# Kernel optimization log

Hardware: AMD Instinct MI355X
Metric: run time of the kernel (lower is better)

The kernel has to match this reference:

```python
import jax, jax.numpy as jnp
import numpy as np


def setup_inputs() -> dict:
    key = jax.random.key(0)
    k1, k2 = jax.random.split(key)
    N = 16384
    NUM_ANCHORS = 64
    HIDDEN_DIM = 128
    adj = jax.random.uniform(k1, (N, N), dtype=jnp.float32)
    anchor_emb = jax.random.normal(k2, (NUM_ANCHORS, HIDDEN_DIM), dtype=jnp.float32)
    return {"adj": adj, "anchor_emb": anchor_emb}


def reference(adj, anchor_emb):
    # adj: [N, N], anchor_emb: [A, H]
    num_anchors = anchor_emb.shape[0]
    deg = jnp.sum(adj, axis=-1, keepdims=True)              # [N, 1]
    nrm = jnp.linalg.norm(deg) + 1e-6                       # scalar ||deg||_F
    # sim[:, :A] of (deg @ deg.T)/nrm computed directly without the full NxN product
    sim = (deg * deg[:num_anchors, 0][None, :]) / nrm       # [N, A]
    anchor_weights = jax.nn.softmax(sim, axis=-1)           # [N, A]
    return anchor_weights @ anchor_emb                      # [N, H]
```

## Files before the change

kernel.cpp:

```cpp
#include <hip/hip_runtime.h>


constexpr int N_NODES = 16384;
constexpr int N_ANCH  = 64;
constexpr int HID     = 128;

__global__ __launch_bounds__(256) void rowsum_kernel(const float* __restrict__ adj,
                                                     float* __restrict__ deg) {
    const int row  = blockIdx.x;
    const int t    = threadIdx.x;
    const float4* __restrict__ p =
        reinterpret_cast<const float4*>(adj) + (size_t)row * (N_NODES / 4);

    float s = 0.0f;
#pragma unroll
    for (int i = 0; i < (N_NODES / 4) / 256; ++i) {
        float4 v = p[t + i * 256];
        s += (v.x + v.y) + (v.z + v.w);
    }
#pragma unroll
    for (int off = 32; off > 0; off >>= 1) s += __shfl_down(s, off, 64);

    __shared__ float partial[4];
    const int lane = t & 63, wid = t >> 6;
    if (lane == 0) partial[wid] = s;
    __syncthreads();
    if (t == 0) deg[row] = (partial[0] + partial[1]) + (partial[2] + partial[3]);
}

__global__ __launch_bounds__(1024) void norm_kernel(const float* __restrict__ deg,
                                                    float* __restrict__ nrm) {
    const int t = threadIdx.x;
    float s = 0.0f;
    for (int i = t; i < N_NODES; i += 1024) {
        float d = deg[i];
        s += d * d;
    }
#pragma unroll
    for (int off = 32; off > 0; off >>= 1) s += __shfl_down(s, off, 64);

    __shared__ float partial[16];
    const int lane = t & 63, wid = t >> 6;
    if (lane == 0) partial[wid] = s;
    __syncthreads();
    if (t == 0) {
        float tot = 0.0f;
#pragma unroll
        for (int i = 0; i < 16; ++i) tot += partial[i];
        *nrm = sqrtf(tot) + 1e-6f;
    }
}

__global__ __launch_bounds__(256) void out_kernel(const float* __restrict__ deg,
                                                  const float* __restrict__ nrm,
                                                  const float* __restrict__ emb,
                                                  float* __restrict__ out) {
    __shared__ float s_emb[N_ANCH * HID];
    __shared__ float s_dega[N_ANCH];

    const int t = threadIdx.x;
    for (int i = t; i < N_ANCH * HID; i += 256) s_emb[i] = emb[i];
    if (t < N_ANCH) s_dega[t] = deg[t];
    __syncthreads();

    const float inv_nrm = 1.0f / (*nrm);
    const int wid = t >> 6, lane = t & 63;
    const int rows_per_wave = N_NODES / (gridDim.x * 4);
    const int row0 = (blockIdx.x * 4 + wid) * rows_per_wave;

    for (int r = 0; r < rows_per_wave; ++r) {
        const int row = row0 + r;
        const float d = deg[row];
        const float sim = d * s_dega[lane] * inv_nrm;

        float m = sim;
#pragma unroll
        for (int off = 32; off > 0; off >>= 1) m = fmaxf(m, __shfl_xor(m, off, 64));
        const float e = expf(sim - m);
        float ssum = e;
#pragma unroll
        for (int off = 32; off > 0; off >>= 1) ssum += __shfl_xor(ssum, off, 64);
        const float w = e / ssum;

        float acc0 = 0.0f, acc1 = 0.0f;
#pragma unroll
        for (int a = 0; a < N_ANCH; ++a) {
            const float wa = __shfl(w, a, 64);
            acc0 = fmaf(wa, s_emb[a * HID + lane],      acc0);
            acc1 = fmaf(wa, s_emb[a * HID + 64 + lane], acc1);
        }
        out[(size_t)row * HID + lane]      = acc0;
        out[(size_t)row * HID + 64 + lane] = acc1;
    }
}

extern "C" void kernel_launch(void* const* d_in, const int* in_sizes, int n_in,
                              void* d_out, int out_size, void* d_ws, size_t ws_size,
                              hipStream_t stream) {
    const float* adj = (const float*)d_in[0];
    const float* emb = (const float*)d_in[1];
    float* out = (float*)d_out;

    float* deg = (float*)d_ws;
    float* nrm = deg + N_NODES;

    rowsum_kernel<<<N_NODES, 256, 0, stream>>>(adj, deg);
    norm_kernel<<<1, 1024, 0, stream>>>(deg, nrm);
    out_kernel<<<1024, 256, 0, stream>>>(deg, nrm, emb, out);
}
```

Before: 219.7 us.

## Fuse norm into rowsum and output kernels, wave-per-row nontemporal loads

Removes the single-block norm kernel. The rowsum kernel now writes per-block partial sums of squares, and the output kernel reduces those partials itself. Rowsum is restructured so each wave handles two rows, with 16 outstanding nontemporal float4 loads per batch to raise memory-level parallelism on the 1 GiB adjacency read. The output kernel keeps embedding columns in registers, passes softmax weights through shared memory instead of per-anchor shuffles, and uses fast exp. In exchange, every output block redundantly reduces the 2048 partials, and register pressure rises.

```diff
diff --git a/kernel.cpp b/kernel.cpp
--- a/kernel.cpp
+++ b/kernel.cpp
@@ -4,90 +4,101 @@
 constexpr int N_NODES = 16384;
 constexpr int N_ANCH  = 64;
 constexpr int HID     = 128;
+constexpr int ROWS_PER_BLOCK = 8;
+constexpr int K1_BLOCKS = N_NODES / ROWS_PER_BLOCK;
+constexpr int K3_BLOCKS = 1024;
+
+typedef float f4 __attribute__((ext_vector_type(4)));
 
 __global__ __launch_bounds__(256) void rowsum_kernel(const float* __restrict__ adj,
-                                                     float* __restrict__ deg) {
-    const int row  = blockIdx.x;
-    const int t    = threadIdx.x;
-    const float4* __restrict__ p =
-        reinterpret_cast<const float4*>(adj) + (size_t)row * (N_NODES / 4);
+                                                     float* __restrict__ deg,
+                                                     float* __restrict__ ssq_part) {
+    const int t = threadIdx.x, lane = t & 63, wid = t >> 6;
+    const int row0 = blockIdx.x * ROWS_PER_BLOCK + wid * 2;
+    float ssq = 0.0f;
 
-    float s = 0.0f;
+    for (int r = 0; r < 2; ++r) {
+        const int row = row0 + r;
+        const f4* __restrict__ p =
+            reinterpret_cast<const f4*>(adj) + (size_t)row * (N_NODES / 4) + lane;
+        float s = 0.0f;
+        for (int c = 0; c < 4; ++c) {
+            f4 v[16];
 #pragma unroll
-    for (int i = 0; i < (N_NODES / 4) / 256; ++i) {
-        float4 v = p[t + i * 256];
-        s += (v.x + v.y) + (v.z + v.w);
+            for (int i = 0; i < 16; ++i)
+                v[i] = __builtin_nontemporal_load(p + c * 1024 + i * 64);
+#pragma unroll
+            for (int i = 0; i < 16; ++i)
+                s += (v[i].x + v[i].y) + (v[i].z + v[i].w);
+        }
+#pragma unroll
+        for (int off = 32; off > 0; off >>= 1) s += __shfl_down(s, off, 64);
+        if (lane == 0) { deg[row] = s; ssq = fmaf(s, s, ssq); }
     }
-#pragma unroll
-    for (int off = 32; off > 0; off >>= 1) s += __shfl_down(s, off, 64);
 
-    __shared__ float partial[4];
-    const int lane = t & 63, wid = t >> 6;
-    if (lane == 0) partial[wid] = s;
+    __shared__ float sp[4];
+    if (lane == 0) sp[wid] = ssq;
     __syncthreads();
-    if (t == 0) deg[row] = (partial[0] + partial[1]) + (partial[2] + partial[3]);
-}
-
-__global__ __launch_bounds__(1024) void norm_kernel(const float* __restrict__ deg,
-                                                    float* __restrict__ nrm) {
-    const int t = threadIdx.x;
-    float s = 0.0f;
-    for (int i = t; i < N_NODES; i += 1024) {
-        float d = deg[i];
-        s += d * d;
-    }
-#pragma unroll
-    for (int off = 32; off > 0; off >>= 1) s += __shfl_down(s, off, 64);
-
-    __shared__ float partial[16];
-    const int lane = t & 63, wid = t >> 6;
-    if (lane == 0) partial[wid] = s;
-    __syncthreads();
-    if (t == 0) {
-        float tot = 0.0f;
-#pragma unroll
-        for (int i = 0; i < 16; ++i) tot += partial[i];
-        *nrm = sqrtf(tot) + 1e-6f;
-    }
+    if (t == 0) ssq_part[blockIdx.x] = (sp[0] + sp[1]) + (sp[2] + sp[3]);
 }
 
 __global__ __launch_bounds__(256) void out_kernel(const float* __restrict__ deg,
-                                                  const float* __restrict__ nrm,
+                                                  const float* __restrict__ ssq_part,
                                                   const float* __restrict__ emb,
                                                   float* __restrict__ out) {
     __shared__ float s_emb[N_ANCH * HID];
-    __shared__ float s_dega[N_ANCH];
+    __shared__ float s_w[4][N_ANCH];
+    __shared__ float s_red[4];
+    __shared__ float s_inv;
 
-    const int t = threadIdx.x;
-    for (int i = t; i < N_ANCH * HID; i += 256) s_emb[i] = emb[i];
-    if (t < N_ANCH) s_dega[t] = deg[t];
+    const int t = threadIdx.x, lane = t & 63, wid = t >> 6;
+
+    float ss = 0.0f;
+#pragma unroll
+    for (int i = 0; i < K1_BLOCKS / 256; ++i) ss += ssq_part[t + i * 256];
+#pragma unroll
+    for (int off = 32; off > 0; off >>= 1) ss += __shfl_down(ss, off, 64);
+    if (lane == 0) s_red[wid] = ss;
+
+    for (int i = t; i < N_ANCH * HID / 4; i += 256)
+        reinterpret_cast<f4*>(s_emb)[i] = reinterpret_cast<const f4*>(emb)[i];
     __syncthreads();
+    if (t == 0)
+        s_inv = 1.0f / (sqrtf((s_red[0] + s_red[1]) + (s_red[2] + s_red[3])) + 1e-6f);
+    __syncthreads();
+    const float inv_nrm = s_inv;
 
-    const float inv_nrm = 1.0f / (*nrm);
-    const int wid = t >> 6, lane = t & 63;
-    const int rows_per_wave = N_NODES / (gridDim.x * 4);
-    const int row0 = (blockIdx.x * 4 + wid) * rows_per_wave;
+    float e0[N_ANCH], e1[N_ANCH];
+#pragma unroll
+    for (int a = 0; a < N_ANCH; ++a) {
+        e0[a] = s_emb[a * HID + lane];
+        e1[a] = s_emb[a * HID + 64 + lane];
+    }
 
-    for (int r = 0; r < rows_per_wave; ++r) {
+    const float da = deg[lane] * inv_nrm;
+    const int row0 = (blockIdx.x * 4 + wid) * 4;
+
+    for (int r = 0; r < 4; ++r) {
         const int row = row0 + r;
-        const float d = deg[row];
-        const float sim = d * s_dega[lane] * inv_nrm;
+        const float sim = deg[row] * da;
 
         float m = sim;
 #pragma unroll
         for (int off = 32; off > 0; off >>= 1) m = fmaxf(m, __shfl_xor(m, off, 64));
-        const float e = expf(sim - m);
-        float ssum = e;
+        const float e = __expf(sim - m);
+        float sum = e;
 #pragma unroll
-        for (int off = 32; off > 0; off >>= 1) ssum += __shfl_xor(ssum, off, 64);
-        const float w = e / ssum;
+        for (int off = 32; off > 0; off >>= 1) sum += __shfl_xor(sum, off, 64);
+        s_w[wid][lane] = e / sum;
 
         float acc0 = 0.0f, acc1 = 0.0f;
 #pragma unroll
-        for (int a = 0; a < N_ANCH; ++a) {
-            const float wa = __shfl(w, a, 64);
-            acc0 = fmaf(wa, s_emb[a * HID + lane],      acc0);
-            acc1 = fmaf(wa, s_emb[a * HID + 64 + lane], acc1);
+        for (int a4 = 0; a4 < N_ANCH; a4 += 4) {
+            f4 w4 = *reinterpret_cast<const f4*>(&s_w[wid][a4]);
+            acc0 = fmaf(w4.x, e0[a4 + 0], acc0); acc1 = fmaf(w4.x, e1[a4 + 0], acc1);
+            acc0 = fmaf(w4.y, e0[a4 + 1], acc0); acc1 = fmaf(w4.y, e1[a4 + 1], acc1);
+            acc0 = fmaf(w4.z, e0[a4 + 2], acc0); acc1 = fmaf(w4.z, e1[a4 + 2], acc1);
+            acc0 = fmaf(w4.w, e0[a4 + 3], acc0); acc1 = fmaf(w4.w, e1[a4 + 3], acc1);
         }
         out[(size_t)row * HID + lane]      = acc0;
         out[(size_t)row * HID + 64 + lane] = acc1;
@@ -101,10 +112,9 @@
     const float* emb = (const float*)d_in[1];
     float* out = (float*)d_out;
 
-    float* deg = (float*)d_ws;
-    float* nrm = deg + N_NODES;
+    float* deg      = (float*)d_ws;
+    float* ssq_part = deg + N_NODES;
 
-    rowsum_kernel<<<N_NODES, 256, 0, stream>>>(adj, deg);
-    norm_kernel<<<1, 1024, 0, stream>>>(deg, nrm);
-    out_kernel<<<1024, 256, 0, stream>>>(deg, nrm, emb, out);
+    rowsum_kernel<<<K1_BLOCKS, 256, 0, stream>>>(adj, deg, ssq_part);
+    out_kernel<<<K3_BLOCKS, 256, 0, stream>>>(deg, ssq_part, emb, out);
 }
```

Result: faster. 180.7 us (-17.8%).
